# Optimization experiments

Measured on AMD Instinct MI355X. Metric: run time of the kernel, lower is better.

## Reference

```python
import jax, jax.numpy as jnp
import numpy as np

N = 100000
E = 800000
D_IN = 64
D_HID = 64
D_OUT = 47


def gcn_conv(x, edge_index, W, b):
    # GCNConv with normalize=False: linear transform then sum-aggregate over edges.
    h = x @ W                              # [N, d_out]
    src, dst = edge_index[0], edge_index[1]
    msg = h[src]                           # [E, d_out] gather
    agg = jax.ops.segment_sum(msg, dst, num_segments=N)  # [N, d_out] scatter-add
    return agg + b


def setup_inputs() -> dict:
    key = jax.random.key(0)
    ks = jax.random.split(key, 8)
    x = jax.random.normal(ks[0], (N, D_IN), dtype=jnp.float32)
    edge_index = jax.random.randint(ks[1], (2, E), 0, N, dtype=jnp.int64)
    # Glorot-ish init for weights, zeros for bias (as in GCNConv.reset_parameters)
    def glorot(k, fan_in, fan_out):
        s = jnp.sqrt(6.0 / (fan_in + fan_out))
        return jax.random.uniform(k, (fan_in, fan_out), jnp.float32, -s, s)
    W1 = glorot(ks[2], D_IN, D_HID)
    b1 = jnp.zeros((D_HID,), jnp.float32)
    W2 = glorot(ks[3], D_HID, D_HID)
    b2 = jnp.zeros((D_HID,), jnp.float32)
    W3 = glorot(ks[4], D_HID, D_OUT)
    b3 = jnp.zeros((D_OUT,), jnp.float32)
    return {"x": x, "edge_index": edge_index,
            "W1": W1, "b1": b1, "W2": W2, "b2": b2, "W3": W3, "b3": b3}


def reference(x, edge_index, W1, b1, W2, b2, W3, b3):
    # Layer 1: conv -> relu (dropout is identity at inference)
    h = jax.nn.relu(gcn_conv(x, edge_index, W1, b1))
    # Layer 2
    h = jax.nn.relu(gcn_conv(h, edge_index, W2, b2))
    # Output layer + log_softmax over classes
    out = gcn_conv(h, edge_index, W3, b3)
    return jax.nn.log_softmax(out, axis=-1)
```

## Files before the change

kernel.cpp:

```cpp
#include <hip/hip_runtime.h>
#include <cmath>


#define SCAN_B 256
#define B1_EPB 4096
#define BKT_SH 8
#define CHUNK  256

typedef __attribute__((ext_vector_type(8))) short bf8;
typedef __attribute__((ext_vector_type(4))) float f4;

__device__ __forceinline__ unsigned int f2bf(float x) {
  unsigned int u = __float_as_uint(x);
  return (u + 0x7FFFu + ((u >> 16) & 1u)) >> 16;
}
__device__ __forceinline__ float bflo(unsigned int u) { return __uint_as_float(u << 16); }
__device__ __forceinline__ float bfhi(unsigned int u) { return __uint_as_float(u & 0xFFFF0000u); }

__global__ void hist_cvt_k(const int* __restrict__ dsti, int* __restrict__ cnt, int ne,
                           const float* __restrict__ x, unsigned short* __restrict__ xb,
                           int n4) {
  int i = blockIdx.x * blockDim.x + threadIdx.x;
  int st = gridDim.x * blockDim.x;
  for (int e = i; e < ne; e += st) atomicAdd(&cnt[dsti[e]], 1);
  for (int j = i; j < n4; j += st) {
    float4 v = ((const float4*)x)[j];
    ushort4 o;
    o.x = (unsigned short)f2bf(v.x); o.y = (unsigned short)f2bf(v.y);
    o.z = (unsigned short)f2bf(v.z); o.w = (unsigned short)f2bf(v.w);
    ((ushort4*)xb)[j] = o;
  }
}

__global__ void scan1_k(int* __restrict__ cnt, int* __restrict__ bsum, int n) {
  __shared__ int sh[SCAN_B];
  int t = threadIdx.x, i = blockIdx.x * SCAN_B + t;
  int x = (i < n) ? cnt[i] : 0;
  sh[t] = x; __syncthreads();
  for (int o = 1; o < SCAN_B; o <<= 1) {
    int v = (t >= o) ? sh[t - o] : 0; __syncthreads();
    sh[t] += v; __syncthreads();
  }
  if (i < n) cnt[i] = sh[t] - x;
  if (t == SCAN_B - 1) bsum[blockIdx.x] = sh[t];
}

__global__ void scan23_k(const int* __restrict__ cnt, const int* __restrict__ bsum,
                         int* __restrict__ row_off, int* __restrict__ bcur,
                         int n, int ne) {
  __shared__ int sh[SCAN_B];
  const int b = blockIdx.x, t = threadIdx.x;
  int s = 0;
  for (int j = t; j < b; j += SCAN_B) s += bsum[j];
  sh[t] = s; __syncthreads();
  for (int o = SCAN_B / 2; o > 0; o >>= 1) {
    if (t < o) sh[t] += sh[t + o];
    __syncthreads();
  }
  const int pref = sh[0];
  const int i = b * SCAN_B + t;
  if (i < n) {
    int v = cnt[i] + pref;
    row_off[i] = v;
    if ((i & ((1 << BKT_SH) - 1)) == 0) bcur[i >> BKT_SH] = v;
  }
  if (b == 0 && t == 0) row_off[n] = ne;
}

__global__ void bucket_k(const int* __restrict__ srci, const int* __restrict__ dsti,
                         int* __restrict__ bcur, uint2* __restrict__ ebuf,
                         int ne, int nbkt) {
  __shared__ int lhist[512], lbase[512];
  const int t = threadIdx.x;
  const int base = blockIdx.x * B1_EPB;
  const int m = min(B1_EPB, ne - base);
  for (int i = t; i < nbkt; i += 256) lhist[i] = 0;
  __syncthreads();
  for (int i = t; i < m; i += 256) atomicAdd(&lhist[dsti[base + i] >> BKT_SH], 1);
  __syncthreads();
  for (int i = t; i < nbkt; i += 256) {
    int c = lhist[i];
    lbase[i] = c ? atomicAdd(&bcur[i], c) : 0;
  }
  __syncthreads();
  for (int i = t; i < nbkt; i += 256) lhist[i] = 0;
  __syncthreads();
  for (int i = t; i < m; i += 256) {
    const int s = srci[base + i], d = dsti[base + i];
    const int b = d >> BKT_SH;
    const int p = lbase[b] + atomicAdd(&lhist[b], 1);
    ebuf[p] = make_uint2((unsigned)s, (unsigned)d);
  }
}

__global__ void fillb_k(const uint2* __restrict__ ebuf, const int* __restrict__ row_off,
                        int* __restrict__ ssrc, int n) {
  __shared__ int lcur[1 << BKT_SH];
  const int b = blockIdx.x, t = threadIdx.x;
  const int v0 = b << BKT_SH;
  const int nv = min(1 << BKT_SH, n - v0);
  if (t < nv) lcur[t] = row_off[v0 + t];
  __syncthreads();
  const int start = row_off[v0];
  const int end   = row_off[v0 + nv];
  for (int i = start + t; i < end; i += 256) {
    const uint2 e = ebuf[i];
    const int p = atomicAdd(&lcur[e.y & ((1 << BKT_SH) - 1)], 1);
    ssrc[p] = (int)e.x;
  }
}

template <int DOUT, bool LS>
__launch_bounds__(256, 4)
__global__ void fused_k(const unsigned short* __restrict__ in,
                        const int* __restrict__ row_off, const int* __restrict__ ssrc,
                        const float* __restrict__ Wm, const float* __restrict__ bin,
                        void* __restrict__ outp, int n) {
  constexpr int NT = (DOUT + 15) / 16;
  const int lane  = threadIdx.x & 63;
  const int wslot = threadIdx.x >> 6;
  const int quad  = lane >> 4;
  const int f16i  = lane & 15;

  __shared__ char rows_raw[4][16 * 144];
  __shared__ int  sidx[4][CHUNK];
  char* my  = rows_raw[wslot];
  int*  sid = sidx[wslot];

  bf8 bfr[2][NT];
#pragma unroll
  for (int s = 0; s < 2; ++s)
#pragma unroll
    for (int t = 0; t < NT; ++t) {
      const int c = t * 16 + f16i;
#pragma unroll
      for (int j = 0; j < 8; ++j) {
        const int k = s * 32 + quad * 8 + j;
        float wv = (c < DOUT) ? Wm[k * DOUT + c] : 0.f;
        bfr[s][t][j] = (short)f2bf(wv);
      }
    }
  float bc[NT];
#pragma unroll
  for (int t = 0; t < NT; ++t) {
    const int c = t * 16 + f16i;
    bc[t] = (c < DOUT) ? bin[c] : 0.f;
  }

  const uint2* in2 = (const uint2*)in;
  const int wid = (int)((blockIdx.x * blockDim.x + threadIdx.x) >> 6);
  const int nwv = (int)((gridDim.x * blockDim.x) >> 6);
  const int ntiles = (n + 15) >> 4;

  for (int tile = wid; tile < ntiles; tile += nwv) {
    const int v0 = tile << 4;
    const int ro_l = row_off[min(v0 + min(lane, 16), n)];
    const int base     = __shfl(ro_l, 0, 64);
    const int tile_end = __shfl(ro_l, 16, 64);
    int ns[4], nE[4];
#pragma unroll
    for (int r = 0; r < 4; ++r) {
      const int m = quad * 4 + r;
      ns[r] = __shfl(ro_l, m, 64);
      nE[r] = __shfl(ro_l, m + 1, 64);
    }

    float4 accA[4], accB[4];
#pragma unroll
    for (int r = 0; r < 4; ++r) {
      accA[r] = make_float4(0.f, 0.f, 0.f, 0.f);
      accB[r] = make_float4(0.f, 0.f, 0.f, 0.f);
    }

    for (int off = base; off < tile_end; off += CHUNK) {
      const int cend = min(tile_end, off + CHUNK);
      const int nL = cend - off;
#pragma unroll
      for (int k = 0; k < CHUNK / 64; ++k) {
        const int p = off + lane + k * 64;
        if (p < cend) sid[lane + k * 64] = ssrc[p];
      }
      asm volatile("s_waitcnt lgkmcnt(0)" ::: "memory");

#pragma unroll
      for (int r = 0; r < 4; ++r) {
        const int ls = max(ns[r], off), le = min(nE[r], cend);
        for (int c = ls; c < le; c += 8) {
          uint2 q[8];
#pragma unroll
          for (int k = 0; k < 8; ++k) {
            const int lofs = min(c - off + k, nL - 1);
            const int s = sid[lofs];
            q[k] = (c + k < le) ? in2[(size_t)s * 16 + f16i]
                                : make_uint2(0u, 0u);
          }
#pragma unroll
          for (int k = 0; k < 8; k += 2) {
            accA[r].x += bflo(q[k].x); accB[r].x += bflo(q[k + 1].x);
            accA[r].y += bfhi(q[k].x); accB[r].y += bfhi(q[k + 1].x);
            accA[r].z += bflo(q[k].y); accB[r].z += bflo(q[k + 1].y);
            accA[r].w += bfhi(q[k].y); accB[r].w += bfhi(q[k + 1].y);
          }
        }
      }
    }

#pragma unroll
    for (int r = 0; r < 4; ++r) {
      const int m = quad * 4 + r;
      uint2 p;
      p.x = f2bf(accA[r].x + accB[r].x) | (f2bf(accA[r].y + accB[r].y) << 16);
      p.y = f2bf(accA[r].z + accB[r].z) | (f2bf(accA[r].w + accB[r].w) << 16);
      *(uint2*)(my + m * 144 + f16i * 8) = p;
    }
    asm volatile("s_waitcnt lgkmcnt(0)" ::: "memory");

    bf8 a0 = *(const bf8*)(my + f16i * 144 + quad * 16);
    bf8 a1 = *(const bf8*)(my + f16i * 144 + quad * 16 + 64);
    f4 acc[NT];
#pragma unroll
    for (int t = 0; t < NT; ++t) {
      f4 z = {0.f, 0.f, 0.f, 0.f};
      acc[t] = __builtin_amdgcn_mfma_f32_16x16x32_bf16(a0, bfr[0][t], z, 0, 0, 0);
      acc[t] = __builtin_amdgcn_mfma_f32_16x16x32_bf16(a1, bfr[1][t], acc[t], 0, 0, 0);
    }

    if (!LS) {
      unsigned short* ob = (unsigned short*)outp;
#pragma unroll
      for (int t = 0; t < NT; ++t)
#pragma unroll
        for (int j = 0; j < 4; ++j) {
          const int v = v0 + quad * 4 + j;
          if (v < n) {
            float val = acc[t][j] + bc[t];
            ob[(size_t)v * 64 + t * 16 + f16i] =
                (unsigned short)f2bf(fmaxf(val, 0.f));
          }
        }
    } else {
      float* ob = (float*)outp;
      float val[NT][4];
#pragma unroll
      for (int t = 0; t < NT; ++t)
#pragma unroll
        for (int j = 0; j < 4; ++j) val[t][j] = acc[t][j] + bc[t];
#pragma unroll
      for (int j = 0; j < 4; ++j) {
        float mx = -INFINITY;
#pragma unroll
        for (int t = 0; t < NT; ++t)
          if (t * 16 + f16i < DOUT) mx = fmaxf(mx, val[t][j]);
#pragma unroll
        for (int o = 1; o <= 8; o <<= 1) mx = fmaxf(mx, __shfl_xor(mx, o, 64));
        float sm = 0.f;
#pragma unroll
        for (int t = 0; t < NT; ++t)
          if (t * 16 + f16i < DOUT) sm += __expf(val[t][j] - mx);
#pragma unroll
        for (int o = 1; o <= 8; o <<= 1) sm += __shfl_xor(sm, o, 64);
        const float lse = mx + __logf(sm);
        const int v = v0 + quad * 4 + j;
        if (v < n) {
#pragma unroll
          for (int t = 0; t < NT; ++t) {
            const int c = t * 16 + f16i;
            if (c < DOUT) ob[(size_t)v * DOUT + c] = val[t][j] - lse;
          }
        }
      }
    }
  }
}

extern "C" void kernel_launch(void* const* d_in, const int* in_sizes, int n_in,
                              void* d_out, int out_size, void* d_ws, size_t ws_size,
                              hipStream_t stream) {
  const float* x  = (const float*)d_in[0];
  const int*   ei = (const int*)d_in[1];
  const float* W1 = (const float*)d_in[2];
  const float* b1 = (const float*)d_in[3];
  const float* W2 = (const float*)d_in[4];
  const float* b2 = (const float*)d_in[5];
  const float* W3 = (const float*)d_in[6];
  const float* b3 = (const float*)d_in[7];
  float* outp = (float*)d_out;

  const int n  = in_sizes[0] / 64;
  const int ne = in_sizes[1] / 2;
  const int* srci = ei;
  const int* dsti = ei + ne;
  const int nbkt = (n + (1 << BKT_SH) - 1) >> BKT_SH;

  const size_t N64 = (size_t)n * 64;
  unsigned short* xb   = (unsigned short*)d_ws;
  unsigned short* bufA = xb + N64;
  unsigned short* bufB = bufA + N64;
  uint2* ebuf   = (uint2*)(bufB + N64);
  int* cnt      = (int*)(ebuf + ne);
  int* row_off  = cnt + n;
  int* bsum     = row_off + n + 1;
  int* bcur     = bsum + 512;
  int* ssrc     = bcur + 512;

  const int TB = 256;
  const int nscan = (n + SCAN_B - 1) / SCAN_B;
  const int b1_blocks = (ne + B1_EPB - 1) / B1_EPB;
  const int fus_blocks = 1568;

  hipMemsetAsync(cnt, 0, (size_t)n * sizeof(int), stream);
  hist_cvt_k<<<2048, TB, 0, stream>>>(dsti, cnt, ne, x, xb, (int)(N64 / 4));
  scan1_k<<<nscan, SCAN_B, 0, stream>>>(cnt, bsum, n);
  scan23_k<<<nscan, SCAN_B, 0, stream>>>(cnt, bsum, row_off, bcur, n, ne);
  bucket_k<<<b1_blocks, TB, 0, stream>>>(srci, dsti, bcur, ebuf, ne, nbkt);
  fillb_k<<<nbkt, TB, 0, stream>>>(ebuf, row_off, ssrc, n);

  fused_k<64, false><<<fus_blocks, TB, 0, stream>>>(xb,   row_off, ssrc, W1, b1, bufA, n);
  fused_k<64, false><<<fus_blocks, TB, 0, stream>>>(bufA, row_off, ssrc, W2, b2, bufB, n);
  fused_k<47, true ><<<fus_blocks, TB, 0, stream>>>(bufB, row_off, ssrc, W3, b3, outp, n);
}
```

Before: 231.8 us.

## Replace global per-node histogram and scans with bucket-level counting sort; unroll gather by 16

The CSR build no longer does a global per-node atomic histogram, a memset and a two-pass scan. Each edge segment now builds a per-bucket histogram in shared memory. A single-block scan yields bucket bases, and fillb_k computes per-node offsets locally with a shared-memory count and scan before scattering. This cuts global atomic contention and removes two kernel launches plus a memset, at the cost of an extra read of ebuf in fillb_k and a serial single-block scan. The aggregation gather loop also issues 16 loads per iteration instead of 8, which raises memory-level parallelism but also register pressure.

Result: slower. 282.4 us (+21.8%).

```diff
diff --git a/kernel.cpp b/kernel.cpp
--- a/kernel.cpp
+++ b/kernel.cpp
@@ -2,7 +2,6 @@
 #include <cmath>
 
 
-#define SCAN_B 256
 #define B1_EPB 4096
 #define BKT_SH 8
 #define CHUNK  256
@@ -17,13 +16,23 @@
 __device__ __forceinline__ float bflo(unsigned int u) { return __uint_as_float(u << 16); }
 __device__ __forceinline__ float bfhi(unsigned int u) { return __uint_as_float(u & 0xFFFF0000u); }
 
-__global__ void hist_cvt_k(const int* __restrict__ dsti, int* __restrict__ cnt, int ne,
-                           const float* __restrict__ x, unsigned short* __restrict__ xb,
-                           int n4) {
-  int i = blockIdx.x * blockDim.x + threadIdx.x;
-  int st = gridDim.x * blockDim.x;
-  for (int e = i; e < ne; e += st) atomicAdd(&cnt[dsti[e]], 1);
-  for (int j = i; j < n4; j += st) {
+__global__ void bhist_cvt_k(const int* __restrict__ dsti, int* __restrict__ part,
+                            int ne, const float* __restrict__ x,
+                            unsigned short* __restrict__ xb, int n4,
+                            int nbkt, int nseg) {
+  __shared__ int lh[512];
+  const int b = blockIdx.x, t = threadIdx.x;
+  if (b < nseg) {
+    for (int i = t; i < nbkt; i += 256) lh[i] = 0;
+    __syncthreads();
+    const int base = b * B1_EPB;
+    const int m = min(B1_EPB, ne - base);
+    for (int i = t; i < m; i += 256) atomicAdd(&lh[dsti[base + i] >> BKT_SH], 1);
+    __syncthreads();
+    for (int i = t; i < nbkt; i += 256) part[b * nbkt + i] = lh[i];
+  }
+  const int gid = b * 256 + t, gst = gridDim.x * 256;
+  for (int j = gid; j < n4; j += gst) {
     float4 v = ((const float4*)x)[j];
     ushort4 o;
     o.x = (unsigned short)f2bf(v.x); o.y = (unsigned short)f2bf(v.y);
@@ -32,39 +41,20 @@
   }
 }
 
-__global__ void scan1_k(int* __restrict__ cnt, int* __restrict__ bsum, int n) {
-  __shared__ int sh[SCAN_B];
-  int t = threadIdx.x, i = blockIdx.x * SCAN_B + t;
-  int x = (i < n) ? cnt[i] : 0;
-  sh[t] = x; __syncthreads();
-  for (int o = 1; o < SCAN_B; o <<= 1) {
+__global__ void bscan_k(const int* __restrict__ part, int* __restrict__ bbase,
+                        int* __restrict__ bcur, int nbkt, int nseg, int ne) {
+  __shared__ int sh[512];
+  const int t = threadIdx.x;
+  int s = 0;
+  if (t < nbkt)
+    for (int b = 0; b < nseg; ++b) s += part[b * nbkt + t];
+  sh[t] = s; __syncthreads();
+  for (int o = 1; o < 512; o <<= 1) {
     int v = (t >= o) ? sh[t - o] : 0; __syncthreads();
     sh[t] += v; __syncthreads();
   }
-  if (i < n) cnt[i] = sh[t] - x;
-  if (t == SCAN_B - 1) bsum[blockIdx.x] = sh[t];
-}
-
-__global__ void scan23_k(const int* __restrict__ cnt, const int* __restrict__ bsum,
-                         int* __restrict__ row_off, int* __restrict__ bcur,
-                         int n, int ne) {
-  __shared__ int sh[SCAN_B];
-  const int b = blockIdx.x, t = threadIdx.x;
-  int s = 0;
-  for (int j = t; j < b; j += SCAN_B) s += bsum[j];
-  sh[t] = s; __syncthreads();
-  for (int o = SCAN_B / 2; o > 0; o >>= 1) {
-    if (t < o) sh[t] += sh[t + o];
-    __syncthreads();
-  }
-  const int pref = sh[0];
-  const int i = b * SCAN_B + t;
-  if (i < n) {
-    int v = cnt[i] + pref;
-    row_off[i] = v;
-    if ((i & ((1 << BKT_SH) - 1)) == 0) bcur[i >> BKT_SH] = v;
-  }
-  if (b == 0 && t == 0) row_off[n] = ne;
+  if (t < nbkt) { int e = sh[t] - s; bbase[t] = e; bcur[t] = e; }
+  if (t == 0) bbase[nbkt] = ne;
 }
 
 __global__ void bucket_k(const int* __restrict__ srci, const int* __restrict__ dsti,
@@ -93,16 +83,29 @@
   }
 }
 
-__global__ void fillb_k(const uint2* __restrict__ ebuf, const int* __restrict__ row_off,
-                        int* __restrict__ ssrc, int n) {
-  __shared__ int lcur[1 << BKT_SH];
+__global__ void fillb_k(const uint2* __restrict__ ebuf, const int* __restrict__ bbase,
+                        int* __restrict__ row_off, int* __restrict__ ssrc,
+                        int n, int ne) {
+  __shared__ int lcnt[256], lpre[256], lcur[256];
   const int b = blockIdx.x, t = threadIdx.x;
   const int v0 = b << BKT_SH;
   const int nv = min(1 << BKT_SH, n - v0);
-  if (t < nv) lcur[t] = row_off[v0 + t];
-  __syncthreads();
-  const int start = row_off[v0];
-  const int end   = row_off[v0 + nv];
+  const int start = bbase[b], end = bbase[b + 1];
+  lcnt[t] = 0; __syncthreads();
+  for (int i = start + t; i < end; i += 256)
+    atomicAdd(&lcnt[ebuf[i].y & ((1 << BKT_SH) - 1)], 1);
+  __syncthreads();
+  const int x = lcnt[t];
+  lpre[t] = x; __syncthreads();
+  for (int o = 1; o < 256; o <<= 1) {
+    int v = (t >= o) ? lpre[t - o] : 0; __syncthreads();
+    lpre[t] += v; __syncthreads();
+  }
+  const int excl = start + lpre[t] - x;
+  lcur[t] = excl;
+  if (t < nv) row_off[v0 + t] = excl;
+  if (t == 0) row_off[v0 + nv] = end;
+  __syncthreads();
   for (int i = start + t; i < end; i += 256) {
     const uint2 e = ebuf[i];
     const int p = atomicAdd(&lcur[e.y & ((1 << BKT_SH) - 1)], 1);
@@ -185,17 +188,17 @@
 #pragma unroll
       for (int r = 0; r < 4; ++r) {
         const int ls = max(ns[r], off), le = min(nE[r], cend);
-        for (int c = ls; c < le; c += 8) {
-          uint2 q[8];
-#pragma unroll
-          for (int k = 0; k < 8; ++k) {
+        for (int c = ls; c < le; c += 16) {
+          uint2 q[16];
+#pragma unroll
+          for (int k = 0; k < 16; ++k) {
             const int lofs = min(c - off + k, nL - 1);
             const int s = sid[lofs];
             q[k] = (c + k < le) ? in2[(size_t)s * 16 + f16i]
                                 : make_uint2(0u, 0u);
           }
 #pragma unroll
-          for (int k = 0; k < 8; k += 2) {
+          for (int k = 0; k < 16; k += 2) {
             accA[r].x += bflo(q[k].x); accB[r].x += bflo(q[k + 1].x);
             accA[r].y += bfhi(q[k].x); accB[r].y += bfhi(q[k + 1].x);
             accA[r].z += bflo(q[k].y); accB[r].z += bflo(q[k + 1].y);
@@ -291,29 +294,26 @@
   const int* srci = ei;
   const int* dsti = ei + ne;
   const int nbkt = (n + (1 << BKT_SH) - 1) >> BKT_SH;
+  const int nseg = (ne + B1_EPB - 1) / B1_EPB;
 
   const size_t N64 = (size_t)n * 64;
   unsigned short* xb   = (unsigned short*)d_ws;
   unsigned short* bufA = xb + N64;
   unsigned short* bufB = bufA + N64;
   uint2* ebuf   = (uint2*)(bufB + N64);
-  int* cnt      = (int*)(ebuf + ne);
-  int* row_off  = cnt + n;
-  int* bsum     = row_off + n + 1;
-  int* bcur     = bsum + 512;
-  int* ssrc     = bcur + 512;
+  int* row_off  = (int*)(ebuf + ne);
+  int* part     = row_off + n + 1;
+  int* bbase    = part + nseg * nbkt;
+  int* bcur     = bbase + nbkt + 1;
+  int* ssrc     = bcur + nbkt;
 
   const int TB = 256;
-  const int nscan = (n + SCAN_B - 1) / SCAN_B;
-  const int b1_blocks = (ne + B1_EPB - 1) / B1_EPB;
   const int fus_blocks = 1568;
 
-  hipMemsetAsync(cnt, 0, (size_t)n * sizeof(int), stream);
-  hist_cvt_k<<<2048, TB, 0, stream>>>(dsti, cnt, ne, x, xb, (int)(N64 / 4));
-  scan1_k<<<nscan, SCAN_B, 0, stream>>>(cnt, bsum, n);
-  scan23_k<<<nscan, SCAN_B, 0, stream>>>(cnt, bsum, row_off, bcur, n, ne);
-  bucket_k<<<b1_blocks, TB, 0, stream>>>(srci, dsti, bcur, ebuf, ne, nbkt);
-  fillb_k<<<nbkt, TB, 0, stream>>>(ebuf, row_off, ssrc, n);
+  bhist_cvt_k<<<784, TB, 0, stream>>>(dsti, part, ne, x, xb, (int)(N64 / 4), nbkt, nseg);
+  bscan_k<<<1, 512, 0, stream>>>(part, bbase, bcur, nbkt, nseg, ne);
+  bucket_k<<<nseg, TB, 0, stream>>>(srci, dsti, bcur, ebuf, ne, nbkt);
+  fillb_k<<<nbkt, TB, 0, stream>>>(ebuf, bbase, row_off, ssrc, n, ne);
 
   fused_k<64, false><<<fus_blocks, TB, 0, stream>>>(xb,   row_off, ssrc, W1, b1, bufA, n);
   fused_k<64, false><<<fus_blocks, TB, 0, stream>>>(bufA, row_off, ssrc, W2, b2, bufB, n);
```
